# Kernel optimization log

Measured on AMD Instinct MI355X. Metric: run time of the kernel, lower is better.

## Reference

```python
import jax, jax.numpy as jnp
import numpy as np

B, N, M, D, H = 4, 512, 4096, 256, 8
HD = D // H


def setup_inputs() -> dict:
    key = jax.random.key(0)
    ks = jax.random.split(key, 10)
    s = 1.0 / np.sqrt(D)
    return {
        "amr_feats": jax.random.normal(ks[0], (B, N, D), jnp.float32),
        "amr_pad_mask": jax.random.randint(ks[1], (B, N), 0, 2) == 1,
        "visual_feats": jax.random.normal(ks[2], (B, M, D), jnp.float32),
        "W_amr_qk": jax.random.normal(ks[3], (D, D), jnp.float32) * s,
        "W_amr_v": jax.random.normal(ks[4], (D, D), jnp.float32) * s,
        "W_vis_qk": jax.random.normal(ks[5], (D, D), jnp.float32) * s,
        "W_vis_v": jax.random.normal(ks[6], (D, D), jnp.float32) * s,
        "W_amr_out": jax.random.normal(ks[7], (D, D), jnp.float32) * s,
        "b_amr_out": jnp.zeros((D,), jnp.float32),
        "W_vis_out": jax.random.normal(ks[8], (D, D), jnp.float32) * s,
        "b_vis_out": jnp.zeros((D,), jnp.float32),
    }


def _split_heads(x):  # [b, s, d] -> [b, h, s, hd]
    b, s, _ = x.shape
    return x.reshape(b, s, H, HD).transpose(0, 2, 1, 3)


def _merge_heads(x):  # [b, h, s, hd] -> [b, s, d]
    b, _, s, _ = x.shape
    return x.transpose(0, 2, 1, 3).reshape(b, s, H * HD)


def reference(amr_feats, amr_pad_mask, visual_feats,
              W_amr_qk, W_amr_v, W_vis_qk, W_vis_v,
              W_amr_out, b_amr_out, W_vis_out, b_vis_out):
    scale = HD ** -0.5
    amr_qk = _split_heads(amr_feats @ W_amr_qk)      # [b,h,n,hd]
    vis_qk = _split_heads(visual_feats @ W_vis_qk)   # [b,h,m,hd]
    amr_v = _split_heads(amr_feats @ W_amr_v)        # [b,h,n,hd]
    vis_v = _split_heads(visual_feats @ W_vis_v)     # [b,h,m,hd]

    # shared score matrix, computed once and reused for both directions
    common = jnp.einsum('bhnc,bhmc->bhnm', amr_qk, vis_qk) * scale  # [b,h,n,m]

    # amr -> visual (visual_pads is None in the top-level forward: no mask)
    amr_vis_w = jax.nn.softmax(common, axis=-1)
    amr_feats_2 = _merge_heads(jnp.einsum('bhnm,bhmc->bhnc', amr_vis_w, vis_v))
    amr_feats_2 = amr_feats_2 @ W_amr_out + b_amr_out

    # visual -> amr, masked by amr_pad_mask
    neg = jnp.finfo(common.dtype).min
    vis_txt = jnp.where(amr_pad_mask[:, None, None, :], neg,
                        common.transpose(0, 1, 3, 2))  # [b,h,m,n]
    vis_txt_w = jax.nn.softmax(vis_txt, axis=-1)
    visual_feats_2 = _merge_heads(jnp.einsum('bhmn,bhnc->bhmc', vis_txt_w, amr_v))
    visual_feats_2 = visual_feats_2 @ W_vis_out + b_vis_out

    # text_trans == 'dot', visual_trans == 'dot'
    return amr_feats_2 * amr_feats, visual_feats * visual_feats_2
```

## Files before the change

kernel.cpp:

```cpp
#include <hip/hip_runtime.h>

#define BB 4
#define NN 512
#define MM 4096
#define DD 256
#define HH 8
#define HDD 32

typedef __attribute__((ext_vector_type(8))) short bf16x8;
typedef __attribute__((ext_vector_type(4))) float f32x4;
typedef __attribute__((ext_vector_type(4))) unsigned int u32x4;

__device__ __forceinline__ unsigned short f2b(float f) {
    union { float f; unsigned u; } v; v.f = f;
    unsigned r = v.u + 0x7fffu + ((v.u >> 16) & 1u);
    return (unsigned short)(r >> 16);
}
__device__ __forceinline__ float b2f(unsigned short u) {
    union { unsigned u; float f; } v; v.u = ((unsigned)u) << 16;
    return v.f;
}
__device__ __forceinline__ unsigned cvt_pk_bf16(float lo, float hi) {
    unsigned r;
    asm("v_cvt_pk_bf16_f32 %0, %1, %2" : "=v"(r) : "v"(lo), "v"(hi));
    return r;
}

struct WPack { const float* s[6]; unsigned short* d[6]; };
__global__ __launch_bounds__(256) void convert_w(WPack p)
{
    __shared__ unsigned short T[64][72];
    const int mat = blockIdx.x >> 4;
    const int tile = blockIdx.x & 15;
    const int kt = (tile >> 2) * 64, ct = (tile & 3) * 64;
    const int t = threadIdx.x;
    const int kl = t >> 2, cseg = (t & 3) * 16;

    const float* src = &p.s[mat][(size_t)(kt + kl) * DD + ct + cseg];
    #pragma unroll
    for (int j4 = 0; j4 < 4; ++j4) {
        const float4 f = *(const float4*)(src + j4 * 4);
        T[cseg + j4 * 4 + 0][kl] = f2b(f.x);
        T[cseg + j4 * 4 + 1][kl] = f2b(f.y);
        T[cseg + j4 * 4 + 2][kl] = f2b(f.z);
        T[cseg + j4 * 4 + 3][kl] = f2b(f.w);
    }
    __syncthreads();
    unsigned short* dst = &p.d[mat][(size_t)(ct + kl) * DD + kt + cseg];
    *(bf16x8*)dst       = *(const bf16x8*)&T[kl][cseg];
    *(bf16x8*)(dst + 8) = *(const bf16x8*)&T[kl][cseg + 8];
}

struct InPack {
    const float* amr; const float* vis;
    const unsigned short *Wqa, *Wva, *Wqv, *Wvv;
    unsigned short *amr_qk, *vis_qk, *VTa, *VTv;
    const int* mask;
    unsigned short* keepP;
    float sqs;
};
__global__ __launch_bounds__(256) void gemm_in(InPack p)
{
    __shared__ unsigned short As[64][72];
    __shared__ unsigned short Wq[64][72];
    __shared__ unsigned short Wv[64][72];

    const int bx = blockIdx.x;
    if (bx == 288) {
        if (blockIdx.y == 0) {
            #pragma unroll
            for (int k8 = 0; k8 < 8; ++k8) {
                const int idx = k8 * 256 + threadIdx.x;
                const int m = idx & (NN - 1);
                const int r = m & 31;
                const int pp = ((r & 15) >> 2) * 8 + (r >> 4) * 4 + (r & 3);
                p.keepP[(idx & ~(NN - 1)) | (m & ~31) | pp]
                    = p.mask[idx] ? (unsigned short)0 : (unsigned short)0x3F80;
            }
        }
        return;
    }

    const float* A; const unsigned short *Wqm, *Wvm;
    unsigned short *Cq, *VT; const int* rowmask; int SEQ, r0;
    if (bx < 32) {
        A = p.amr; Wqm = p.Wqa; Wvm = p.Wva; Cq = p.amr_qk; VT = p.VTa;
        rowmask = p.mask; SEQ = NN; r0 = bx * 64;
    } else {
        A = p.vis; Wqm = p.Wqv; Wvm = p.Wvv; Cq = p.vis_qk; VT = p.VTv;
        rowmask = nullptr; SEQ = MM; r0 = (bx - 32) * 64;
    }
    const int c0 = blockIdx.y * 64;

    const int tid = threadIdx.x;
    const int lane = tid & 63, w = tid >> 6;
    const int rq = (w >> 1) * 32, cq = (w & 1) * 32;
    const int srow = tid >> 2, skc = (tid & 3) * 16;
    const int g = lane >> 4, cl = lane & 15;

    f32x4 aq[2][2] = {};
    f32x4 av[2][2] = {};

    for (int ks = 0; ks < DD; ks += 64) {
        __syncthreads();
        {
            const float* ga = &A[(size_t)(r0 + srow) * DD + ks + skc];
            const float4 f0 = *(const float4*)(ga);
            const float4 f1 = *(const float4*)(ga + 4);
            const float4 f2 = *(const float4*)(ga + 8);
            const float4 f3 = *(const float4*)(ga + 12);
            uint4 u0, u1;
            u0.x = cvt_pk_bf16(f0.x, f0.y); u0.y = cvt_pk_bf16(f0.z, f0.w);
            u0.z = cvt_pk_bf16(f1.x, f1.y); u0.w = cvt_pk_bf16(f1.z, f1.w);
            u1.x = cvt_pk_bf16(f2.x, f2.y); u1.y = cvt_pk_bf16(f2.z, f2.w);
            u1.z = cvt_pk_bf16(f3.x, f3.y); u1.w = cvt_pk_bf16(f3.z, f3.w);
            *(uint4*)&As[srow][skc]     = u0;
            *(uint4*)&As[srow][skc + 8] = u1;
            const unsigned short* gq = &Wqm[(size_t)(c0 + srow) * DD + ks + skc];
            *(bf16x8*)&Wq[srow][skc]     = *(const bf16x8*)gq;
            *(bf16x8*)&Wq[srow][skc + 8] = *(const bf16x8*)(gq + 8);
            const unsigned short* gv = &Wvm[(size_t)(c0 + srow) * DD + ks + skc];
            *(bf16x8*)&Wv[srow][skc]     = *(const bf16x8*)gv;
            *(bf16x8*)&Wv[srow][skc + 8] = *(const bf16x8*)(gv + 8);
        }
        __syncthreads();
        #pragma unroll
        for (int kh = 0; kh < 2; ++kh) {
            const int kk = kh * 32 + g * 8;
            const bf16x8 a0 = *(const bf16x8*)&As[rq + cl][kk];
            const bf16x8 a1 = *(const bf16x8*)&As[rq + 16 + cl][kk];
            const bf16x8 q0 = *(const bf16x8*)&Wq[cq + cl][kk];
            const bf16x8 q1 = *(const bf16x8*)&Wq[cq + 16 + cl][kk];
            const bf16x8 v0 = *(const bf16x8*)&Wv[cq + cl][kk];
            const bf16x8 v1 = *(const bf16x8*)&Wv[cq + 16 + cl][kk];
            aq[0][0] = __builtin_amdgcn_mfma_f32_16x16x32_bf16(a0, q0, aq[0][0], 0, 0, 0);
            aq[0][1] = __builtin_amdgcn_mfma_f32_16x16x32_bf16(a0, q1, aq[0][1], 0, 0, 0);
            aq[1][0] = __builtin_amdgcn_mfma_f32_16x16x32_bf16(a1, q0, aq[1][0], 0, 0, 0);
            aq[1][1] = __builtin_amdgcn_mfma_f32_16x16x32_bf16(a1, q1, aq[1][1], 0, 0, 0);
            av[0][0] = __builtin_amdgcn_mfma_f32_16x16x32_bf16(a0, v0, av[0][0], 0, 0, 0);
            av[0][1] = __builtin_amdgcn_mfma_f32_16x16x32_bf16(a0, v1, av[0][1], 0, 0, 0);
            av[1][0] = __builtin_amdgcn_mfma_f32_16x16x32_bf16(a1, v0, av[1][0], 0, 0, 0);
            av[1][1] = __builtin_amdgcn_mfma_f32_16x16x32_bf16(a1, v1, av[1][1], 0, 0, 0);
        }
    }

    const int b0 = r0 / SEQ, mbase = r0 % SEQ;

    #pragma unroll
    for (int sr = 0; sr < 2; ++sr)
    #pragma unroll
    for (int sc = 0; sc < 2; ++sc) {
        const int col = c0 + cq + sc * 16 + cl;
        const int head = col >> 5, c32 = col & 31;
        #pragma unroll
        for (int reg = 0; reg < 4; ++reg) {
            const int m = mbase + rq + sr * 16 + g * 4 + reg;
            Cq[(((size_t)b0 * HH + head) * SEQ + m) * 32 + c32]
                = f2b(aq[sr][sc][reg] * p.sqs);
        }
    }

    if (rowmask != nullptr) {
        #pragma unroll
        for (int sr = 0; sr < 2; ++sr)
            #pragma unroll
            for (int reg = 0; reg < 4; ++reg) {
                const int m = mbase + rq + sr * 16 + g * 4 + reg;
                const float k = rowmask[b0 * SEQ + m] ? 0.f : 1.f;
                av[sr][0][reg] *= k;
                av[sr][1][reg] *= k;
            }
    }
    __syncthreads();
    #pragma unroll
    for (int sr = 0; sr < 2; ++sr)
    #pragma unroll
    for (int sc = 0; sc < 2; ++sc) {
        const int col_local = cq + sc * 16 + cl;
        uint2 u;
        u.x = cvt_pk_bf16(av[sr][sc][0], av[sr][sc][1]);
        u.y = cvt_pk_bf16(av[sr][sc][2], av[sr][sc][3]);
        *(uint2*)&As[col_local][rq + g * 8 + sr * 4] = u;
    }
    __syncthreads();
    {
        const int col = tid >> 2, seg = tid & 3;
        unsigned short* dst = &VT[((size_t)b0 * DD + c0 + col) * SEQ + mbase + seg * 16];
        *(bf16x8*)dst       = *(const bf16x8*)&As[col][seg * 16];
        *(bf16x8*)(dst + 8) = *(const bf16x8*)&As[col][seg * 16 + 8];
    }
}

__device__ __forceinline__ void gemm_tile_out(
    const unsigned short* __restrict__ A,
    const unsigned short* __restrict__ Wt,
    const float* __restrict__ bias,
    const float* __restrict__ feats,
    float* __restrict__ Cf,
    int r0, int c0,
    unsigned short (*As)[72], unsigned short (*Ws)[72])
{
    const int tid = threadIdx.x;
    const int lane = tid & 63, w = tid >> 6;
    const int rq = (w >> 1) * 32, cq = (w & 1) * 32;
    const int srow = tid >> 2, skc = (tid & 3) * 16;
    const int g = lane >> 4, cl = lane & 15;

    f32x4 acc[2][2] = {};

    for (int ks = 0; ks < DD; ks += 64) {
        __syncthreads();
        {
            const unsigned short* ga = &A[(size_t)(r0 + srow) * DD + ks + skc];
            *(bf16x8*)&As[srow][skc]     = *(const bf16x8*)ga;
            *(bf16x8*)&As[srow][skc + 8] = *(const bf16x8*)(ga + 8);
            const unsigned short* gw = &Wt[(size_t)(c0 + srow) * DD + ks + skc];
            *(bf16x8*)&Ws[srow][skc]     = *(const bf16x8*)gw;
            *(bf16x8*)&Ws[srow][skc + 8] = *(const bf16x8*)(gw + 8);
        }
        __syncthreads();
        #pragma unroll
        for (int kh = 0; kh < 2; ++kh) {
            const int kk = kh * 32 + g * 8;
            const bf16x8 a0 = *(const bf16x8*)&As[rq + cl][kk];
            const bf16x8 a1 = *(const bf16x8*)&As[rq + 16 + cl][kk];
            const bf16x8 b0 = *(const bf16x8*)&Ws[cq + cl][kk];
            const bf16x8 b1 = *(const bf16x8*)&Ws[cq + 16 + cl][kk];
            acc[0][0] = __builtin_amdgcn_mfma_f32_16x16x32_bf16(a0, b0, acc[0][0], 0, 0, 0);
            acc[0][1] = __builtin_amdgcn_mfma_f32_16x16x32_bf16(a0, b1, acc[0][1], 0, 0, 0);
            acc[1][0] = __builtin_amdgcn_mfma_f32_16x16x32_bf16(a1, b0, acc[1][0], 0, 0, 0);
            acc[1][1] = __builtin_amdgcn_mfma_f32_16x16x32_bf16(a1, b1, acc[1][1], 0, 0, 0);
        }
    }

    #pragma unroll
    for (int sr = 0; sr < 2; ++sr)
    #pragma unroll
    for (int sc = 0; sc < 2; ++sc) {
        const int col = c0 + cq + sc * 16 + cl;
        #pragma unroll
        for (int reg = 0; reg < 4; ++reg) {
            const int row = r0 + rq + sr * 16 + g * 4 + reg;
            const size_t idx = (size_t)row * DD + col;
            Cf[idx] = (acc[sr][sc][reg] + bias[col]) * feats[idx];
        }
    }
}

struct OutPack {
    const unsigned short* A[2];
    const unsigned short* Wt[2];
    const float* bias[2];
    const float* feats[2];
    float* O[2];
};
__global__ __launch_bounds__(256) void gemm_out(OutPack p)
{
    __shared__ unsigned short As[64][72];
    __shared__ unsigned short Ws[64][72];
    const int bx = blockIdx.x;
    const int which = (bx < 32) ? 0 : 1;
    const int rb = (bx < 32) ? bx : bx - 32;
    gemm_tile_out(p.A[which], p.Wt[which], p.bias[which], p.feats[which],
                  p.O[which], rb * 64, blockIdx.y * 64, As, Ws);
}

template<int SEQK, int SPLIT, bool HAS_KEEP>
__device__ __forceinline__ void attn_body(
    int bid,
    const unsigned short* __restrict__ Qb,
    const unsigned short* __restrict__ Kb,
    const unsigned short* __restrict__ VTb,
    const unsigned short* __restrict__ keepP,
    unsigned short* __restrict__ ctx,
    float* __restrict__ Pl, unsigned short* __restrict__ PaccB,
    int NQ)
{
    constexpr int KCHUNK = SEQK / SPLIT;
    constexpr int NT = KCHUNK / 64;

    const int tid = threadIdx.x;
    const int lane = tid & 63, w = tid >> 6;
    const int g = lane >> 4, cl = lane & 15;

    const int nqt = NQ / 256;
    int bi = bid;
    const int sp = bi % SPLIT; bi /= SPLIT;
    const int qt = bi % nqt;   bi /= nqt;
    const int h  = bi % HH;
    const int b  = bi / HH;
    const int q0 = qt * 256 + w * 64;
    const int kv0 = sp * KCHUNK;

    bf16x8 aq[4];
    #pragma unroll
    for (int qg = 0; qg < 4; ++qg)
        aq[qg] = *(const bf16x8*)
            &Qb[(((size_t)b * HH + h) * NQ + q0 + qg * 16 + cl) * 32 + g * 8];

    const unsigned short* Kp0 = Kb + (((size_t)b * HH + h) * SEQK + kv0 + cl) * 32 + g * 8;
    const unsigned short* Vp0 = VTb + ((size_t)b * DD + h * HDD + cl) * SEQK + kv0 + g * 8;
    const unsigned short* Op0 = HAS_KEEP ? (keepP + (size_t)b * SEQK + kv0 + g * 8) : nullptr;

    union { u32x4 u; bf16x8 b; } onesc;
    onesc.u[0] = 0x3F803F80u; onesc.u[1] = 0x3F803F80u;
    onesc.u[2] = 0x3F803F80u; onesc.u[3] = 0x3F803F80u;

    f32x4 acc[4][2] = {};
    f32x4 acc_l[4] = {};

    bf16x8 Kc[4], Kn[4];
    #pragma unroll
    for (int kf = 0; kf < 4; ++kf)
        Kc[kf] = *(const bf16x8*)(Kp0 + (size_t)(kf * 16) * 32);

    for (int t = 0; t < NT; ++t) {
        if (t + 1 < NT) {
            const unsigned short* kp = Kp0 + (size_t)((t + 1) * 64) * 32;
            #pragma unroll
            for (int kf = 0; kf < 4; ++kf)
                Kn[kf] = *(const bf16x8*)(kp + (size_t)(kf * 16) * 32);
        }

        bf16x8 vv[2][2];
        #pragma unroll
        for (int mh = 0; mh < 2; ++mh)
            #pragma unroll
            for (int sub = 0; sub < 2; ++sub)
                vv[mh][sub] = *(const bf16x8*)
                    (Vp0 + (size_t)(sub * 16) * SEQK + t * 64 + mh * 32);

        bf16x8 ofrag[2];
        if (HAS_KEEP) {
            ofrag[0] = *(const bf16x8*)(Op0 + t * 64);
            ofrag[1] = *(const bf16x8*)(Op0 + t * 64 + 32);
        } else {
            ofrag[0] = onesc.b;
            ofrag[1] = onesc.b;
        }

        uint2 X[4][4];
        #pragma unroll
        for (int kh = 0; kh < 2; ++kh) {
            f32x4 s[4][2];
            #pragma unroll
            for (int k2 = 0; k2 < 2; ++k2) {
                const f32x4 z = {0.f, 0.f, 0.f, 0.f};
                const bf16x8 kfrag = Kc[kh * 2 + k2];
                #pragma unroll
                for (int qg = 0; qg < 4; ++qg)
                    s[qg][k2] = __builtin_amdgcn_mfma_f32_16x16x32_bf16(
                        kfrag, aq[qg], z, 0, 0, 0);
            }
            #pragma unroll
            for (int k2 = 0; k2 < 2; ++k2) {
                const int kf = kh * 2 + k2;
                #pragma unroll
                for (int qg = 0; qg < 4; ++qg) {
                    const float p0 = exp2f(s[qg][k2][0]);
                    const float p1 = exp2f(s[qg][k2][1]);
                    const float p2 = exp2f(s[qg][k2][2]);
                    const float p3 = exp2f(s[qg][k2][3]);
                    X[qg][kf].x = cvt_pk_bf16(p0, p1);
                    X[qg][kf].y = cvt_pk_bf16(p2, p3);
                }
            }
        }

        #pragma unroll
        for (int mh = 0; mh < 2; ++mh) {
            union { u32x4 u; bf16x8 b; } pa[4];
            #pragma unroll
            for (int qg = 0; qg < 4; ++qg) {
                pa[qg].u[0] = X[qg][mh * 2].x;
                pa[qg].u[1] = X[qg][mh * 2].y;
                pa[qg].u[2] = X[qg][mh * 2 + 1].x;
                pa[qg].u[3] = X[qg][mh * 2 + 1].y;
            }
            #pragma unroll
            for (int sub = 0; sub < 2; ++sub)
                #pragma unroll
                for (int qg = 0; qg < 4; ++qg)
                    acc[qg][sub] = __builtin_amdgcn_mfma_f32_16x16x32_bf16(
                        pa[qg].b, vv[mh][sub], acc[qg][sub], 0, 0, 0);
            #pragma unroll
            for (int qg = 0; qg < 4; ++qg)
                acc_l[qg] = __builtin_amdgcn_mfma_f32_16x16x32_bf16(
                    pa[qg].b, ofrag[mh], acc_l[qg], 0, 0, 0);
        }

        #pragma unroll
        for (int kf = 0; kf < 4; ++kf) Kc[kf] = Kn[kf];
    }

    if (SPLIT > 1) {
        const int pb = bid;
        #pragma unroll
        for (int qg = 0; qg < 4; ++qg) {
            #pragma unroll
            for (int sub = 0; sub < 2; ++sub)
                #pragma unroll
                for (int reg = 0; reg < 4; ++reg) {
                    const int wq = w * 64 + qg * 16 + g * 4 + reg;
                    PaccB[((size_t)pb * 256 + wq) * 32 + sub * 16 + cl]
                        = f2b(acc[qg][sub][reg]);
                }
            if (cl == 0) {
                #pragma unroll
                for (int reg = 0; reg < 4; ++reg)
                    Pl[(size_t)pb * 256 + w * 64 + qg * 16 + g * 4 + reg]
                        = acc_l[qg][reg];
            }
        }
    } else {
        #pragma unroll
        for (int qg = 0; qg < 4; ++qg)
            #pragma unroll
            for (int sub = 0; sub < 2; ++sub)
                #pragma unroll
                for (int reg = 0; reg < 4; ++reg) {
                    const int q = q0 + qg * 16 + g * 4 + reg;
                    ctx[((size_t)b * NQ + q) * DD + h * HDD + sub * 16 + cl]
                        = f2b(acc[qg][sub][reg] / acc_l[qg][reg]);
                }
    }
}

__global__ __launch_bounds__(256) void attn_fused(
    const unsigned short* __restrict__ amr_qk,
    const unsigned short* __restrict__ vis_qk,
    const unsigned short* __restrict__ VT_vis,
    const unsigned short* __restrict__ VT_amr,
    const unsigned short* __restrict__ keepP,
    unsigned short* __restrict__ ctx1,
    float* __restrict__ Pl, unsigned short* __restrict__ PaccB)
{
    if ((blockIdx.x & 1) == 0) {
        attn_body<MM, 8, false>(blockIdx.x >> 1, amr_qk, vis_qk, VT_vis, nullptr,
                                nullptr, Pl, PaccB, NN);
    } else {
        attn_body<NN, 1, true>(blockIdx.x >> 1, vis_qk, amr_qk, VT_amr, keepP,
                               ctx1, nullptr, nullptr, MM);
    }
}

__global__ __launch_bounds__(256) void combine_split(
    const float* __restrict__ Pl, const unsigned short* __restrict__ PaccB,
    unsigned short* __restrict__ ctx)
{
    const int q = threadIdx.x;
    const int bqt = blockIdx.x;
    const int qt = bqt & 1, h = (bqt >> 1) & 7, b = bqt >> 4;
    const int pb0 = bqt * 8;

    float denom = 0.f;
    float o[32] = {};
    #pragma unroll
    for (int sp = 0; sp < 8; ++sp) {
        const size_t base = ((size_t)(pb0 + sp) * 256 + q) * 32;
        #pragma unroll
        for (int c8 = 0; c8 < 4; ++c8) {
            const bf16x8 a = *(const bf16x8*)&PaccB[base + c8 * 8];
            #pragma unroll
            for (int j = 0; j < 8; ++j)
                o[c8 * 8 + j] += b2f((unsigned short)a[j]);
        }
        denom += Pl[(size_t)(pb0 + sp) * 256 + q];
    }
    const float inv = 1.f / denom;

    unsigned short* dst = &ctx[((size_t)b * NN + qt * 256 + q) * DD + h * HDD];
    #pragma unroll
    for (int j4 = 0; j4 < 8; ++j4) {
        ushort4 u;
        u.x = f2b(o[j4 * 4 + 0] * inv); u.y = f2b(o[j4 * 4 + 1] * inv);
        u.z = f2b(o[j4 * 4 + 2] * inv); u.w = f2b(o[j4 * 4 + 3] * inv);
        *(ushort4*)(dst + j4 * 4) = u;
    }
}

extern "C" void kernel_launch(void* const* d_in, const int* in_sizes, int n_in,
                              void* d_out, int out_size, void* d_ws, size_t ws_size,
                              hipStream_t stream)
{
    const float* amr_feats    = (const float*)d_in[0];
    const int*   amr_pad_mask = (const int*)d_in[1];
    const float* visual_feats = (const float*)d_in[2];
    const float* W_amr_qk     = (const float*)d_in[3];
    const float* W_amr_v      = (const float*)d_in[4];
    const float* W_vis_qk     = (const float*)d_in[5];
    const float* W_vis_v      = (const float*)d_in[6];
    const float* W_amr_out    = (const float*)d_in[7];
    const float* b_amr_out    = (const float*)d_in[8];
    const float* W_vis_out    = (const float*)d_in[9];
    const float* b_vis_out    = (const float*)d_in[10];

    unsigned short* ws = (unsigned short*)d_ws;
    unsigned short* Wt_amr_qk  = ws;
    unsigned short* Wt_amr_v   = ws + 65536;
    unsigned short* Wt_vis_qk  = ws + 131072;
    unsigned short* Wt_vis_v   = ws + 196608;
    unsigned short* Wt_amr_out = ws + 262144;
    unsigned short* Wt_vis_out = ws + 327680;
    unsigned short* amr_qk_b   = ws + 393216;
    unsigned short* VT_amr     = ws + 917504;
    unsigned short* vis_qk_b   = ws + 1441792;
    unsigned short* VT_vis     = ws + 5636096;
    unsigned short* ctx0_b     = ws + 9830400;
    unsigned short* ctx1_b     = ws + 10354688;
    float* Pl                  = (float*)(ws + 14548992);
    unsigned short* PaccB      = ws + 15073280;
    unsigned short* keepP      = ws + 19267584;

    float* out0 = (float*)d_out;
    float* out1 = out0 + (size_t)BB * NN * DD;

    const float SQS = 0.50500976f;

    WPack wp;
    wp.s[0] = W_amr_qk;  wp.d[0] = Wt_amr_qk;
    wp.s[1] = W_amr_v;   wp.d[1] = Wt_amr_v;
    wp.s[2] = W_vis_qk;  wp.d[2] = Wt_vis_qk;
    wp.s[3] = W_vis_v;   wp.d[3] = Wt_vis_v;
    wp.s[4] = W_amr_out; wp.d[4] = Wt_amr_out;
    wp.s[5] = W_vis_out; wp.d[5] = Wt_vis_out;
    convert_w<<<96, 256, 0, stream>>>(wp);

    InPack ip;
    ip.amr = amr_feats; ip.vis = visual_feats;
    ip.Wqa = Wt_amr_qk; ip.Wva = Wt_amr_v;
    ip.Wqv = Wt_vis_qk; ip.Wvv = Wt_vis_v;
    ip.amr_qk = amr_qk_b; ip.vis_qk = vis_qk_b;
    ip.VTa = VT_amr; ip.VTv = VT_vis;
    ip.mask = amr_pad_mask; ip.keepP = keepP;
    ip.sqs = SQS;
    gemm_in<<<dim3(289, 4), 256, 0, stream>>>(ip);

    attn_fused<<<1024, 256, 0, stream>>>(
        amr_qk_b, vis_qk_b, VT_vis, VT_amr, keepP, ctx1_b, Pl, PaccB);
    combine_split<<<64, 256, 0, stream>>>(Pl, PaccB, ctx0_b);

    OutPack op;
    op.A[0] = ctx0_b; op.Wt[0] = Wt_amr_out; op.bias[0] = b_amr_out;
    op.feats[0] = amr_feats;    op.O[0] = out0;
    op.A[1] = ctx1_b; op.Wt[1] = Wt_vis_out; op.bias[1] = b_vis_out;
    op.feats[1] = visual_feats; op.O[1] = out1;
    gemm_out<<<dim3(288, 4), 256, 0, stream>>>(op);
}
```

Measured before the change: 88.55 us.

## Restructure input projection GEMM to load full activation row block once per workgroup

The input projection kernel now uses 512-thread workgroups, each covering a 64-row block across all 256 output columns. The whole fp32 activation row block is converted to bf16 once into shared memory instead of being reloaded for each of four column tiles. Weight fragments are now read directly from global memory (L2/L1) rather than staged through shared memory. This cuts redundant activation loads and conversions, but uncoalesced weight reads and fewer, larger blocks could hurt latency hiding.

```diff
diff --git a/kernel.cpp b/kernel.cpp
--- a/kernel.cpp
+++ b/kernel.cpp
@@ -59,24 +59,23 @@
     unsigned short* keepP;
     float sqs;
 };
-__global__ __launch_bounds__(256) void gemm_in(InPack p)
-{
-    __shared__ unsigned short As[64][72];
-    __shared__ unsigned short Wq[64][72];
-    __shared__ unsigned short Wv[64][72];
+__global__ __launch_bounds__(512) void gemm_in(InPack p)
+{
+    __shared__ unsigned short Asl[64][264];
+    __shared__ unsigned short Vr[2][64][72];
 
     const int bx = blockIdx.x;
+    const int tid = threadIdx.x;
+
     if (bx == 288) {
-        if (blockIdx.y == 0) {
-            #pragma unroll
-            for (int k8 = 0; k8 < 8; ++k8) {
-                const int idx = k8 * 256 + threadIdx.x;
-                const int m = idx & (NN - 1);
-                const int r = m & 31;
-                const int pp = ((r & 15) >> 2) * 8 + (r >> 4) * 4 + (r & 3);
-                p.keepP[(idx & ~(NN - 1)) | (m & ~31) | pp]
-                    = p.mask[idx] ? (unsigned short)0 : (unsigned short)0x3F80;
-            }
+        #pragma unroll
+        for (int k4 = 0; k4 < 4; ++k4) {
+            const int idx = k4 * 512 + tid;
+            const int m = idx & (NN - 1);
+            const int r = m & 31;
+            const int pp = ((r & 15) >> 2) * 8 + (r >> 4) * 4 + (r & 3);
+            p.keepP[(idx & ~(NN - 1)) | (m & ~31) | pp]
+                = p.mask[idx] ? (unsigned short)0 : (unsigned short)0x3F80;
         }
         return;
     }
@@ -90,104 +89,99 @@
         A = p.vis; Wqm = p.Wqv; Wvm = p.Wvv; Cq = p.vis_qk; VT = p.VTv;
         rowmask = nullptr; SEQ = MM; r0 = (bx - 32) * 64;
     }
-    const int c0 = blockIdx.y * 64;
-
-    const int tid = threadIdx.x;
+    const int b0 = r0 / SEQ, mbase = r0 % SEQ;
+
+    {
+        const int row = tid >> 3, k0 = (tid & 7) * 32;
+        const float* ga = &A[(size_t)(r0 + row) * DD + k0];
+        #pragma unroll
+        for (int j = 0; j < 4; ++j) {
+            const float4 f0 = *(const float4*)(ga + j * 8);
+            const float4 f1 = *(const float4*)(ga + j * 8 + 4);
+            uint4 u;
+            u.x = cvt_pk_bf16(f0.x, f0.y); u.y = cvt_pk_bf16(f0.z, f0.w);
+            u.z = cvt_pk_bf16(f1.x, f1.y); u.w = cvt_pk_bf16(f1.z, f1.w);
+            *(uint4*)&Asl[row][k0 + j * 8] = u;
+        }
+    }
+    __syncthreads();
+
     const int lane = tid & 63, w = tid >> 6;
-    const int rq = (w >> 1) * 32, cq = (w & 1) * 32;
-    const int srow = tid >> 2, skc = (tid & 3) * 16;
+    const int half = w >> 2, w2 = w & 3;
+    const int rq = (w2 >> 1) * 32, cq = (w2 & 1) * 32;
     const int g = lane >> 4, cl = lane & 15;
 
-    f32x4 aq[2][2] = {};
-    f32x4 av[2][2] = {};
-
-    for (int ks = 0; ks < DD; ks += 64) {
+    #pragma unroll
+    for (int cth = 0; cth < 2; ++cth) {
+        const int ct = half * 2 + cth;
+        const int c0 = ct * 64;
+
+        f32x4 aqc[2][2] = {};
+        f32x4 avc[2][2] = {};
+        const unsigned short* Wqp = &Wqm[(size_t)(c0 + cq + cl) * DD + g * 8];
+        const unsigned short* Wvp = &Wvm[(size_t)(c0 + cq + cl) * DD + g * 8];
+
+        #pragma unroll
+        for (int ks = 0; ks < DD; ks += 32) {
+            const bf16x8 a0 = *(const bf16x8*)&Asl[rq + cl][ks + g * 8];
+            const bf16x8 a1 = *(const bf16x8*)&Asl[rq + 16 + cl][ks + g * 8];
+            const bf16x8 q0 = *(const bf16x8*)(Wqp + ks);
+            const bf16x8 q1 = *(const bf16x8*)(Wqp + (size_t)16 * DD + ks);
+            const bf16x8 v0 = *(const bf16x8*)(Wvp + ks);
+            const bf16x8 v1 = *(const bf16x8*)(Wvp + (size_t)16 * DD + ks);
+            aqc[0][0] = __builtin_amdgcn_mfma_f32_16x16x32_bf16(a0, q0, aqc[0][0], 0, 0, 0);
+            aqc[0][1] = __builtin_amdgcn_mfma_f32_16x16x32_bf16(a0, q1, aqc[0][1], 0, 0, 0);
+            aqc[1][0] = __builtin_amdgcn_mfma_f32_16x16x32_bf16(a1, q0, aqc[1][0], 0, 0, 0);
+            aqc[1][1] = __builtin_amdgcn_mfma_f32_16x16x32_bf16(a1, q1, aqc[1][1], 0, 0, 0);
+            avc[0][0] = __builtin_amdgcn_mfma_f32_16x16x32_bf16(a0, v0, avc[0][0], 0, 0, 0);
+            avc[0][1] = __builtin_amdgcn_mfma_f32_16x16x32_bf16(a0, v1, avc[0][1], 0, 0, 0);
+            avc[1][0] = __builtin_amdgcn_mfma_f32_16x16x32_bf16(a1, v0, avc[1][0], 0, 0, 0);
+            avc[1][1] = __builtin_amdgcn_mfma_f32_16x16x32_bf16(a1, v1, avc[1][1], 0, 0, 0);
+        }
+
+        #pragma unroll
+        for (int sr = 0; sr < 2; ++sr)
+        #pragma unroll
+        for (int sc = 0; sc < 2; ++sc) {
+            const int col = c0 + cq + sc * 16 + cl;
+            const int head = col >> 5, c32 = col & 31;
+            #pragma unroll
+            for (int reg = 0; reg < 4; ++reg) {
+                const int m = mbase + rq + sr * 16 + g * 4 + reg;
+                Cq[(((size_t)b0 * HH + head) * SEQ + m) * 32 + c32]
+                    = f2b(aqc[sr][sc][reg] * p.sqs);
+            }
+        }
+
+        if (rowmask != nullptr) {
+            #pragma unroll
+            for (int sr = 0; sr < 2; ++sr)
+                #pragma unroll
+                for (int reg = 0; reg < 4; ++reg) {
+                    const int m = mbase + rq + sr * 16 + g * 4 + reg;
+                    const float k = rowmask[b0 * SEQ + m] ? 0.f : 1.f;
+                    avc[sr][0][reg] *= k;
+                    avc[sr][1][reg] *= k;
+                }
+        }
+        __syncthreads();
+        #pragma unroll
+        for (int sr = 0; sr < 2; ++sr)
+        #pragma unroll
+        for (int sc = 0; sc < 2; ++sc) {
+            const int col_local = cq + sc * 16 + cl;
+            uint2 u;
+            u.x = cvt_pk_bf16(avc[sr][sc][0], avc[sr][sc][1]);
+            u.y = cvt_pk_bf16(avc[sr][sc][2], avc[sr][sc][3]);
+            *(uint2*)&Vr[half][col_local][rq + g * 8 + sr * 4] = u;
+        }
         __syncthreads();
         {
-            const float* ga = &A[(size_t)(r0 + srow) * DD + ks + skc];
-            const float4 f0 = *(const float4*)(ga);
-            const float4 f1 = *(const float4*)(ga + 4);
-            const float4 f2 = *(const float4*)(ga + 8);
-            const float4 f3 = *(const float4*)(ga + 12);
-            uint4 u0, u1;
-            u0.x = cvt_pk_bf16(f0.x, f0.y); u0.y = cvt_pk_bf16(f0.z, f0.w);
-            u0.z = cvt_pk_bf16(f1.x, f1.y); u0.w = cvt_pk_bf16(f1.z, f1.w);
-            u1.x = cvt_pk_bf16(f2.x, f2.y); u1.y = cvt_pk_bf16(f2.z, f2.w);
-            u1.z = cvt_pk_bf16(f3.x, f3.y); u1.w = cvt_pk_bf16(f3.z, f3.w);
-            *(uint4*)&As[srow][skc]     = u0;
-            *(uint4*)&As[srow][skc + 8] = u1;
-            const unsigned short* gq = &Wqm[(size_t)(c0 + srow) * DD + ks + skc];
-            *(bf16x8*)&Wq[srow][skc]     = *(const bf16x8*)gq;
-            *(bf16x8*)&Wq[srow][skc + 8] = *(const bf16x8*)(gq + 8);
-            const unsigned short* gv = &Wvm[(size_t)(c0 + srow) * DD + ks + skc];
-            *(bf16x8*)&Wv[srow][skc]     = *(const bf16x8*)gv;
-            *(bf16x8*)&Wv[srow][skc + 8] = *(const bf16x8*)(gv + 8);
-        }
-        __syncthreads();
-        #pragma unroll
-        for (int kh = 0; kh < 2; ++kh) {
-            const int kk = kh * 32 + g * 8;
-            const bf16x8 a0 = *(const bf16x8*)&As[rq + cl][kk];
-            const bf16x8 a1 = *(const bf16x8*)&As[rq + 16 + cl][kk];
-            const bf16x8 q0 = *(const bf16x8*)&Wq[cq + cl][kk];
-            const bf16x8 q1 = *(const bf16x8*)&Wq[cq + 16 + cl][kk];
-            const bf16x8 v0 = *(const bf16x8*)&Wv[cq + cl][kk];
-            const bf16x8 v1 = *(const bf16x8*)&Wv[cq + 16 + cl][kk];
-            aq[0][0] = __builtin_amdgcn_mfma_f32_16x16x32_bf16(a0, q0, aq[0][0], 0, 0, 0);
-            aq[0][1] = __builtin_amdgcn_mfma_f32_16x16x32_bf16(a0, q1, aq[0][1], 0, 0, 0);
-            aq[1][0] = __builtin_amdgcn_mfma_f32_16x16x32_bf16(a1, q0, aq[1][0], 0, 0, 0);
-            aq[1][1] = __builtin_amdgcn_mfma_f32_16x16x32_bf16(a1, q1, aq[1][1], 0, 0, 0);
-            av[0][0] = __builtin_amdgcn_mfma_f32_16x16x32_bf16(a0, v0, av[0][0], 0, 0, 0);
-            av[0][1] = __builtin_amdgcn_mfma_f32_16x16x32_bf16(a0, v1, av[0][1], 0, 0, 0);
-            av[1][0] = __builtin_amdgcn_mfma_f32_16x16x32_bf16(a1, v0, av[1][0], 0, 0, 0);
-            av[1][1] = __builtin_amdgcn_mfma_f32_16x16x32_bf16(a1, v1, av[1][1], 0, 0, 0);
-        }
-    }
-
-    const int b0 = r0 / SEQ, mbase = r0 % SEQ;
-
-    #pragma unroll
-    for (int sr = 0; sr < 2; ++sr)
-    #pragma unroll
-    for (int sc = 0; sc < 2; ++sc) {
-        const int col = c0 + cq + sc * 16 + cl;
-        const int head = col >> 5, c32 = col & 31;
-        #pragma unroll
-        for (int reg = 0; reg < 4; ++reg) {
-            const int m = mbase + rq + sr * 16 + g * 4 + reg;
-            Cq[(((size_t)b0 * HH + head) * SEQ + m) * 32 + c32]
-                = f2b(aq[sr][sc][reg] * p.sqs);
-        }
-    }
-
-    if (rowmask != nullptr) {
-        #pragma unroll
-        for (int sr = 0; sr < 2; ++sr)
-            #pragma unroll
-            for (int reg = 0; reg < 4; ++reg) {
-                const int m = mbase + rq + sr * 16 + g * 4 + reg;
-                const float k = rowmask[b0 * SEQ + m] ? 0.f : 1.f;
-                av[sr][0][reg] *= k;
-                av[sr][1][reg] *= k;
-            }
-    }
-    __syncthreads();
-    #pragma unroll
-    for (int sr = 0; sr < 2; ++sr)
-    #pragma unroll
-    for (int sc = 0; sc < 2; ++sc) {
-        const int col_local = cq + sc * 16 + cl;
-        uint2 u;
-        u.x = cvt_pk_bf16(av[sr][sc][0], av[sr][sc][1]);
-        u.y = cvt_pk_bf16(av[sr][sc][2], av[sr][sc][3]);
-        *(uint2*)&As[col_local][rq + g * 8 + sr * 4] = u;
-    }
-    __syncthreads();
-    {
-        const int col = tid >> 2, seg = tid & 3;
-        unsigned short* dst = &VT[((size_t)b0 * DD + c0 + col) * SEQ + mbase + seg * 16];
-        *(bf16x8*)dst       = *(const bf16x8*)&As[col][seg * 16];
-        *(bf16x8*)(dst + 8) = *(const bf16x8*)&As[col][seg * 16 + 8];
+            const int col = (tid & 255) >> 2, seg = tid & 3;
+            unsigned short* dst = &VT[((size_t)b0 * DD + c0 + col) * SEQ + mbase + seg * 16];
+            *(bf16x8*)dst       = *(const bf16x8*)&Vr[half][col][seg * 16];
+            *(bf16x8*)(dst + 8) = *(const bf16x8*)&Vr[half][col][seg * 16 + 8];
+        }
     }
 }
 
@@ -534,7 +528,7 @@
     ip.VTa = VT_amr; ip.VTv = VT_vis;
     ip.mask = amr_pad_mask; ip.keepP = keepP;
     ip.sqs = SQS;
-    gemm_in<<<dim3(289, 4), 256, 0, stream>>>(ip);
+    gemm_in<<<289, 512, 0, stream>>>(ip);
 
     attn_fused<<<1024, 256, 0, stream>>>(
         amr_qk_b, vis_qk_b, VT_vis, VT_amr, keepP, ctx1_b, Pl, PaccB);
```

Measured after the change: 108.2 us. +22.1%, slower.
